# Kernel tuning notes

Measured on AMD Instinct MI355X. Metric: run time of the kernel, lower is better.

The kernel has to match this reference:

```python
import jax, jax.numpy as jnp
import numpy as np

NUM_HEADS = 8


def setup_inputs() -> dict:
    key = jax.random.key(0)
    ks = jax.random.split(key, 5)
    B, N, D = 2, 2048, 512
    scale = 1.0 / np.sqrt(D)  # xavier-ish init for stability
    return {
        "x": jax.random.normal(ks[0], (B, N, D), dtype=jnp.float32),
        "Wq": jax.random.normal(ks[1], (D, D), dtype=jnp.float32) * scale,
        "Wk": jax.random.normal(ks[2], (D, D), dtype=jnp.float32) * scale,
        "Wv": jax.random.normal(ks[3], (D, D), dtype=jnp.float32) * scale,
        "Wo": jax.random.normal(ks[4], (D, D), dtype=jnp.float32) * scale,
        "log_c": jnp.zeros((), dtype=jnp.float32),
        "log_beta": jnp.zeros((), dtype=jnp.float32),
    }


def reference(x, Wq, Wk, Wv, Wo, log_c, log_beta):
    B, N, D = x.shape
    H = NUM_HEADS
    dh = D // H

    # torch nn.Linear: y = x @ W.T
    def proj(W):
        return (x @ W.T).reshape(B, N, H, dh).transpose(0, 2, 1, 3)  # [B,H,N,dh]

    q, k, v = proj(Wq), proj(Wk), proj(Wv)

    c = jax.nn.softplus(log_c)
    beta = jax.nn.softplus(log_beta) + 0.5

    q_nsq = jnp.sum(q * q, axis=-1)  # [B,H,N]
    k_nsq = jnp.sum(k * k, axis=-1)  # [B,H,N]
    qk = jnp.einsum("bhnd,bhmd->bhnm", q, k)  # [B,H,N,N]

    diff_sq = jnp.maximum(q_nsq[..., :, None] - 2.0 * qk + k_nsq[..., None, :], 0.0)
    hyp_factor = jnp.sqrt(1.0 + c * (q_nsq[..., :, None] + k_nsq[..., None, :]))
    dist = jnp.sqrt(diff_sq + 1e-8) * hyp_factor
    scores = -beta * dist

    # causal mask (original: causal = mask is not None)
    causal = jnp.tril(jnp.ones((N, N), dtype=bool))
    scores = jnp.where(causal, scores, -jnp.inf)

    p = jax.nn.softmax(scores, axis=-1)
    out = jnp.einsum("bhnm,bhmd->bhnd", p, v)  # [B,H,N,dh]
    out = out.transpose(0, 2, 1, 3).reshape(B, N, D)
    return out @ Wo.T
```

## Files before the change

### kernel.cpp

```cpp
#include <hip/hip_runtime.h>
#include <math.h>

#define BB   2
#define NN   2048
#define DDIM 512
#define HH   8
#define DH   64
#define MTOT (BB*NN)
#define LDK  72
#define EE   (BB*HH*NN*DH)
#define WN   (DDIM*DDIM)
#define NSLOT (BB*HH*32*4)

typedef __attribute__((ext_vector_type(8))) short bf16x8;
typedef __attribute__((ext_vector_type(4))) float f32x4;

__device__ __forceinline__ float softplus_f(float x) {
    return x > 20.f ? x : log1pf(expf(x));
}
__device__ __forceinline__ unsigned short f2bf(float x) {
    union { float f; unsigned u; } v; v.f = x;
    unsigned r = v.u + 0x7fffu + ((v.u >> 16) & 1u);
    return (unsigned short)(r >> 16);
}
__device__ __forceinline__ float bf2f(unsigned short h) {
    union { unsigned u; float f; } v; v.u = ((unsigned)h) << 16; return v.f;
}

__global__ __launch_bounds__(256)
void split_hl(const float* __restrict__ x,  const float* __restrict__ Wq,
              const float* __restrict__ Wk, const float* __restrict__ Wv,
              const float* __restrict__ Wo,
              unsigned short* __restrict__ xh,  unsigned short* __restrict__ xl,
              unsigned short* __restrict__ wqh, unsigned short* __restrict__ wql,
              unsigned short* __restrict__ wkh, unsigned short* __restrict__ wkl,
              unsigned short* __restrict__ wvh, unsigned short* __restrict__ wvl,
              unsigned short* __restrict__ woh, unsigned short* __restrict__ wol)
{
    const float* src; unsigned short *dh, *dl; int nq;
    switch (blockIdx.y) {
        case 0:  src = x;  dh = xh;  dl = xl;  nq = EE / 4; break;
        case 1:  src = Wq; dh = wqh; dl = wql; nq = WN / 4; break;
        case 2:  src = Wk; dh = wkh; dl = wkl; nq = WN / 4; break;
        case 3:  src = Wv; dh = wvh; dl = wvl; nq = WN / 4; break;
        default: src = Wo; dh = woh; dl = wol; nq = WN / 4; break;
    }
    for (int i = blockIdx.x * 256 + threadIdx.x; i < nq; i += gridDim.x * 256) {
        float4 v = *(const float4*)(src + 4 * (size_t)i);
        ushort4 h, l;
        h.x = f2bf(v.x); l.x = f2bf(v.x - bf2f(h.x));
        h.y = f2bf(v.y); l.y = f2bf(v.y - bf2f(h.y));
        h.z = f2bf(v.z); l.z = f2bf(v.z - bf2f(h.z));
        h.w = f2bf(v.w); l.w = f2bf(v.w - bf2f(h.w));
        *(ushort4*)(dh + 4 * (size_t)i) = h;
        *(ushort4*)(dl + 4 * (size_t)i) = l;
    }
}

__global__ __launch_bounds__(256)
void mm_mfma(const unsigned short* __restrict__ Ahg, const unsigned short* __restrict__ Alg,
             const unsigned short* __restrict__ W0h, const unsigned short* __restrict__ W0l,
             const unsigned short* __restrict__ W1h, const unsigned short* __restrict__ W1l,
             const unsigned short* __restrict__ W2h, const unsigned short* __restrict__ W2l,
             const int is_out,
             unsigned short* __restrict__ Qhi, unsigned short* __restrict__ Qlo,
             unsigned short* __restrict__ Khi, unsigned short* __restrict__ Klo,
             unsigned short* __restrict__ Vb, float* __restrict__ Outp,
             float* __restrict__ QN, float* __restrict__ KN)
{
    const int mode = is_out ? 3 : (int)blockIdx.z;
    const unsigned short* Wh = (mode == 1) ? W1h : ((mode == 2) ? W2h : W0h);
    const unsigned short* Wl = (mode == 1) ? W1l : ((mode == 2) ? W2l : W0l);
    const int m0 = blockIdx.x * 128, n0 = blockIdx.y * 128;

    __shared__ unsigned short Ah_s[4 * 128 * 8];
    __shared__ unsigned short Al_s[4 * 128 * 8];
    __shared__ unsigned short Bh_s[4 * 128 * 8];
    __shared__ unsigned short Bl_s[4 * 128 * 8];

    const int tid  = threadIdx.x;
    const int lane = tid & 63, lx = lane & 15, q4 = lane >> 4;
    const int w = tid >> 6, wm = w & 1, wn = w >> 1;
    const int srow = tid & 127, skh = tid >> 7;

    f32x4 acc[4][4];
    #pragma unroll
    for (int mt = 0; mt < 4; ++mt)
        #pragma unroll
        for (int nt = 0; nt < 4; ++nt)
            acc[mt][nt] = (f32x4){0.f, 0.f, 0.f, 0.f};

    const int am = m0 + srow;
    const int ab = am >> 11, an = am & 2047;
    const size_t brow = (size_t)(n0 + srow) * DDIM;

    uint4 ra0, ra1, ra2, ra3, rb0, rb1, rb2, rb3;
    {
        const int e = skh * 16;
        size_t aoff = (mode == 3)
            ? ((((size_t)(ab * HH + (e >> 6)) * NN + an) << 6) + (e & 63))
            : ((size_t)am * DDIM + e);
        ra0 = *(const uint4*)(Ahg + aoff);     ra1 = *(const uint4*)(Ahg + aoff + 8);
        ra2 = *(const uint4*)(Alg + aoff);     ra3 = *(const uint4*)(Alg + aoff + 8);
        rb0 = *(const uint4*)(Wh + brow + e);  rb1 = *(const uint4*)(Wh + brow + e + 8);
        rb2 = *(const uint4*)(Wl + brow + e);  rb3 = *(const uint4*)(Wl + brow + e + 8);
    }

    for (int k0 = 0; k0 < DDIM; k0 += 32) {
        __syncthreads();
        const int kq = skh * 2;
        *(uint4*)&Ah_s[((kq + 0) * 128 + srow) * 8] = ra0;
        *(uint4*)&Ah_s[((kq + 1) * 128 + srow) * 8] = ra1;
        *(uint4*)&Al_s[((kq + 0) * 128 + srow) * 8] = ra2;
        *(uint4*)&Al_s[((kq + 1) * 128 + srow) * 8] = ra3;
        *(uint4*)&Bh_s[((kq + 0) * 128 + srow) * 8] = rb0;
        *(uint4*)&Bh_s[((kq + 1) * 128 + srow) * 8] = rb1;
        *(uint4*)&Bl_s[((kq + 0) * 128 + srow) * 8] = rb2;
        *(uint4*)&Bl_s[((kq + 1) * 128 + srow) * 8] = rb3;
        __syncthreads();

        if (k0 + 32 < DDIM) {
            const int e = k0 + 32 + skh * 16;
            size_t aoff = (mode == 3)
                ? ((((size_t)(ab * HH + (e >> 6)) * NN + an) << 6) + (e & 63))
                : ((size_t)am * DDIM + e);
            ra0 = *(const uint4*)(Ahg + aoff);     ra1 = *(const uint4*)(Ahg + aoff + 8);
            ra2 = *(const uint4*)(Alg + aoff);     ra3 = *(const uint4*)(Alg + aoff + 8);
            rb0 = *(const uint4*)(Wh + brow + e);  rb1 = *(const uint4*)(Wh + brow + e + 8);
            rb2 = *(const uint4*)(Wl + brow + e);  rb3 = *(const uint4*)(Wl + brow + e + 8);
        }

        bf16x8 fah[4], fal[4], fbh[4], fbl[4];
        #pragma unroll
        for (int t = 0; t < 4; ++t) {
            fah[t] = *(const bf16x8*)&Ah_s[(q4 * 128 + wm * 64 + t * 16 + lx) * 8];
            fal[t] = *(const bf16x8*)&Al_s[(q4 * 128 + wm * 64 + t * 16 + lx) * 8];
            fbh[t] = *(const bf16x8*)&Bh_s[(q4 * 128 + wn * 64 + t * 16 + lx) * 8];
            fbl[t] = *(const bf16x8*)&Bl_s[(q4 * 128 + wn * 64 + t * 16 + lx) * 8];
        }
        #pragma unroll
        for (int mt = 0; mt < 4; ++mt)
            #pragma unroll
            for (int nt = 0; nt < 4; ++nt) {
                acc[mt][nt] = __builtin_amdgcn_mfma_f32_16x16x32_bf16(fah[mt], fbh[nt], acc[mt][nt], 0, 0, 0);
                acc[mt][nt] = __builtin_amdgcn_mfma_f32_16x16x32_bf16(fah[mt], fbl[nt], acc[mt][nt], 0, 0, 0);
                acc[mt][nt] = __builtin_amdgcn_mfma_f32_16x16x32_bf16(fal[mt], fbh[nt], acc[mt][nt], 0, 0, 0);
            }
    }

    if (mode == 0 || mode == 1) {
        float* Np = (mode == 0) ? QN : KN;
        const int head = (n0 + wn * 64) >> 6;
        #pragma unroll
        for (int mt = 0; mt < 4; ++mt)
            #pragma unroll
            for (int r = 0; r < 4; ++r) {
                float s = 0.f;
                #pragma unroll
                for (int nt = 0; nt < 4; ++nt) s = fmaf(acc[mt][nt][r], acc[mt][nt][r], s);
                s += __shfl_xor(s, 1);
                s += __shfl_xor(s, 2);
                s += __shfl_xor(s, 4);
                s += __shfl_xor(s, 8);
                if (lx == 0) {
                    const int m = m0 + wm * 64 + mt * 16 + q4 * 4 + r;
                    Np[(size_t)((m >> 11) * HH + head) * NN + (m & 2047)] = s;
                }
            }
    }

    #pragma unroll
    for (int mt = 0; mt < 4; ++mt) {
        #pragma unroll
        for (int r = 0; r < 4; ++r) {
            const int m = m0 + wm * 64 + mt * 16 + q4 * 4 + r;
            const int b = m >> 11, n2 = m & 2047;
            #pragma unroll
            for (int nt = 0; nt < 4; ++nt) {
                const int j = n0 + wn * 64 + nt * 16 + lx;
                const float v = acc[mt][nt][r];
                if (mode == 3) {
                    Outp[(size_t)m * DDIM + j] = v;
                } else {
                    const size_t idx = (((size_t)(b * HH + (j >> 6)) * NN + n2) << 6) + (j & 63);
                    if (mode == 2) {
                        Vb[idx] = f2bf(v);
                    } else {
                        const unsigned short h = f2bf(v);
                        const unsigned short l = f2bf(v - bf2f(h));
                        if (mode == 0) { Qhi[idx] = h; Qlo[idx] = l; }
                        else           { Khi[idx] = h; Klo[idx] = l; }
                    }
                }
            }
        }
    }
}

__global__ __launch_bounds__(256)
void v_transpose(const unsigned short* __restrict__ Vb, unsigned short* __restrict__ Vt)
{
    __shared__ unsigned short T[64 * LDK];
    const int id = blockIdx.x;
    const int bh = id >> 5, nt = id & 31;
    const size_t ibase = (((size_t)bh * NN + nt * 64) << 6);
    const int row = threadIdx.x >> 2, ch = threadIdx.x & 3;

    #pragma unroll
    for (int half = 0; half < 2; ++half) {
        const int col = ch * 8 + half * 32;
        *(uint4*)&T[row * LDK + col] = *(const uint4*)(Vb + ibase + (row << 6) + col);
    }
    __syncthreads();

    const size_t obase = (size_t)bh * 64 * NN;
    #pragma unroll
    for (int half = 0; half < 2; ++half) {
        const int col = ch * 8 + half * 32;
        union { unsigned short u[8]; uint4 v; } tmp;
        #pragma unroll
        for (int j = 0; j < 8; ++j) tmp.u[j] = T[(col + j) * LDK + row];
        *(uint4*)(Vt + obase + (size_t)row * NN + nt * 64 + col) = tmp.v;
    }
}

__global__ __launch_bounds__(256, 2)
void attn_mfma(const unsigned short* __restrict__ Qhi, const unsigned short* __restrict__ Qlo,
               const unsigned short* __restrict__ Khi, const unsigned short* __restrict__ Klo,
               const unsigned short* __restrict__ Vt,
               const float* __restrict__ QN, const float* __restrict__ KN,
               const float* __restrict__ pLC, const float* __restrict__ pLB,
               float* __restrict__ Opart, float* __restrict__ Mp, float* __restrict__ Lp)
{
    __shared__ unsigned short Kh_s[64 * LDK];
    __shared__ unsigned short Kl_s[64 * LDK];
    __shared__ unsigned short Vt_s[64 * LDK];
    __shared__ unsigned short P_s [64 * LDK];
    __shared__ float kn_s[64];
    __shared__ float qn_s[64];

    const int idx = blockIdx.x;
    const int g   = (idx >= 48) ? 3 : (idx >= 24) ? 2 : (idx >= 8) ? 1 : 0;
    const int rem = idx - 4 * g * (g + 1);
    const int qt  = g * 8 + rem / (g + 1);
    const int c0  = rem % (g + 1);
    const int bh  = blockIdx.y;
    const int kt0 = c0 * 8;
    const int kend = min(kt0 + 8, qt + 1);

    const int tid  = threadIdx.x;
    const int w    = tid >> 6;
    const int lane = tid & 63;
    const int lx   = lane & 15;
    const int q4   = lane >> 4;

    const float hc   = softplus_f(pLC[0]);
    const float beta = softplus_f(pLB[0]) + 0.5f;

    const size_t base = ((size_t)bh * NN) << 6;

    const unsigned short* qrh = Qhi + base + ((size_t)(qt * 64 + w * 16 + lx) << 6) + q4 * 8;
    const unsigned short* qrl = Qlo + base + ((size_t)(qt * 64 + w * 16 + lx) << 6) + q4 * 8;
    const bf16x8 qh0 = *(const bf16x8*)(qrh);
    const bf16x8 qh1 = *(const bf16x8*)(qrh + 32);
    const bf16x8 ql0 = *(const bf16x8*)(qrl);
    const bf16x8 ql1 = *(const bf16x8*)(qrl + 32);

    if (tid < 64) qn_s[tid] = QN[(size_t)bh * NN + qt * 64 + tid];

    f32x4 Oacc[4];
    float m_st[4], l_st[4];
    #pragma unroll
    for (int r = 0; r < 4; ++r) {
        m_st[r] = -INFINITY; l_st[r] = 0.f;
        Oacc[r] = (f32x4){0.f, 0.f, 0.f, 0.f};
    }

    const int srow = tid >> 2, sch = tid & 3;

    uint4 pKh0, pKh1, pKl0, pKl1, pVt0, pVt1; float pkn = 0.f;
    {
        const unsigned short* kh = Khi + base + ((size_t)(kt0 * 64 + srow) << 6);
        const unsigned short* kl = Klo + base + ((size_t)(kt0 * 64 + srow) << 6);
        const unsigned short* vt = Vt  + base + (size_t)srow * NN + kt0 * 64;
        pKh0 = *(const uint4*)(kh + sch * 8);  pKh1 = *(const uint4*)(kh + sch * 8 + 32);
        pKl0 = *(const uint4*)(kl + sch * 8);  pKl1 = *(const uint4*)(kl + sch * 8 + 32);
        pVt0 = *(const uint4*)(vt + sch * 8);  pVt1 = *(const uint4*)(vt + sch * 8 + 32);
        if (tid < 64) pkn = KN[(size_t)bh * NN + kt0 * 64 + tid];
    }

    __syncthreads();

    for (int kt = kt0; kt < kend; ++kt) {
        *(uint4*)&Kh_s[srow * LDK + sch * 8]      = pKh0;
        *(uint4*)&Kh_s[srow * LDK + sch * 8 + 32] = pKh1;
        *(uint4*)&Kl_s[srow * LDK + sch * 8]      = pKl0;
        *(uint4*)&Kl_s[srow * LDK + sch * 8 + 32] = pKl1;
        *(uint4*)&Vt_s[srow * LDK + sch * 8]      = pVt0;
        *(uint4*)&Vt_s[srow * LDK + sch * 8 + 32] = pVt1;
        if (tid < 64) kn_s[tid] = pkn;
        __syncthreads();

        if (kt + 1 < kend) {
            const unsigned short* kh = Khi + base + ((size_t)((kt + 1) * 64 + srow) << 6);
            const unsigned short* kl = Klo + base + ((size_t)((kt + 1) * 64 + srow) << 6);
            const unsigned short* vt = Vt  + base + (size_t)srow * NN + (kt + 1) * 64;
            pKh0 = *(const uint4*)(kh + sch * 8);  pKh1 = *(const uint4*)(kh + sch * 8 + 32);
            pKl0 = *(const uint4*)(kl + sch * 8);  pKl1 = *(const uint4*)(kl + sch * 8 + 32);
            pVt0 = *(const uint4*)(vt + sch * 8);  pVt1 = *(const uint4*)(vt + sch * 8 + 32);
            if (tid < 64) pkn = KN[(size_t)bh * NN + (kt + 1) * 64 + tid];
        }

        f32x4 S[4];
        #pragma unroll
        for (int t = 0; t < 4; ++t) {
            f32x4 acc = (f32x4){0.f, 0.f, 0.f, 0.f};
            #pragma unroll
            for (int c2 = 0; c2 < 2; ++c2) {
                const int off = (t * 16 + lx) * LDK + c2 * 32 + q4 * 8;
                const bf16x8 kh = *(const bf16x8*)&Kh_s[off];
                const bf16x8 kl = *(const bf16x8*)&Kl_s[off];
                const bf16x8 qh = c2 ? qh1 : qh0;
                const bf16x8 ql = c2 ? ql1 : ql0;
                acc = __builtin_amdgcn_mfma_f32_16x16x32_bf16(qh, kh, acc, 0, 0, 0);
                acc = __builtin_amdgcn_mfma_f32_16x16x32_bf16(qh, kl, acc, 0, 0, 0);
                acc = __builtin_amdgcn_mfma_f32_16x16x32_bf16(ql, kh, acc, 0, 0, 0);
            }
            S[t] = acc;
        }

        float qn_r[4];
        #pragma unroll
        for (int r = 0; r < 4; ++r) qn_r[r] = qn_s[w * 16 + q4 * 4 + r];
        const bool diag = (kt == qt);

        float mrow[4] = {-INFINITY, -INFINITY, -INFINITY, -INFINITY};
        #pragma unroll
        for (int t = 0; t < 4; ++t) {
            const float kn = kn_s[t * 16 + lx];
            #pragma unroll
            for (int r = 0; r < 4; ++r) {
                const float sumn = qn_r[r] + kn;
                float diff = fmaxf(fmaf(-2.f, S[t][r], sumn), 0.f);
                float s = -beta * sqrtf(fmaf(hc, sumn, 1.f) * (diff + 1e-8f));
                const int cc = t * 16 + lx;
                const int rr = w * 16 + q4 * 4 + r;
                if (diag && cc > rr) s = -INFINITY;
                S[t][r] = s;
                mrow[r] = fmaxf(mrow[r], s);
            }
        }

        #pragma unroll
        for (int r = 0; r < 4; ++r) {
            float m = mrow[r];
            m = fmaxf(m, __shfl_xor(m, 1));
            m = fmaxf(m, __shfl_xor(m, 2));
            m = fmaxf(m, __shfl_xor(m, 4));
            m = fmaxf(m, __shfl_xor(m, 8));
            const float mn = fmaxf(m_st[r], m);
            const float al = __expf(m_st[r] - mn);
            m_st[r] = mn;
            float rs = 0.f;
            #pragma unroll
            for (int t = 0; t < 4; ++t) {
                const float p = __expf(S[t][r] - mn);
                rs += p;
                P_s[(w * 16 + q4 * 4 + r) * LDK + t * 16 + lx] = f2bf(p);
            }
            rs += __shfl_xor(rs, 1);
            rs += __shfl_xor(rs, 2);
            rs += __shfl_xor(rs, 4);
            rs += __shfl_xor(rs, 8);
            l_st[r] = l_st[r] * al + rs;
            #pragma unroll
            for (int t = 0; t < 4; ++t) Oacc[t][r] *= al;
        }

        __builtin_amdgcn_wave_barrier();

        #pragma unroll
        for (int c2 = 0; c2 < 2; ++c2) {
            const bf16x8 pa = *(const bf16x8*)&P_s[(w * 16 + lx) * LDK + c2 * 32 + q4 * 8];
            #pragma unroll
            for (int t = 0; t < 4; ++t) {
                const bf16x8 vb = *(const bf16x8*)&Vt_s[(t * 16 + lx) * LDK + c2 * 32 + q4 * 8];
                Oacc[t] = __builtin_amdgcn_mfma_f32_16x16x32_bf16(pa, vb, Oacc[t], 0, 0, 0);
            }
        }
        __syncthreads();
    }

    const int slot = ((bh * 32 + qt) << 2) + c0;
    float* op = Opart + ((size_t)slot << 12);
    #pragma unroll
    for (int r = 0; r < 4; ++r) {
        const int row = w * 16 + q4 * 4 + r;
        #pragma unroll
        for (int t = 0; t < 4; ++t)
            op[row * 64 + t * 16 + lx] = Oacc[t][r];
        if (lx == 0) {
            Mp[slot * 64 + row] = m_st[r];
            Lp[slot * 64 + row] = l_st[r];
        }
    }
}

__global__ __launch_bounds__(256)
void attn_combine(const float* __restrict__ Opart, const float* __restrict__ Mp,
                  const float* __restrict__ Lp,
                  unsigned short* __restrict__ AOh, unsigned short* __restrict__ AOl)
{
    const int bh = blockIdx.x >> 5, qt = blockIdx.x & 31;
    const int C = (qt >> 3) + 1;
    const int row = threadIdx.x >> 2, qd = threadIdx.x & 3;
    const int slot0 = (bh * 32 + qt) << 2;

    float m = -INFINITY;
    for (int c = 0; c < C; ++c) m = fmaxf(m, Mp[(slot0 + c) * 64 + row]);
    float L = 0.f;
    float o[16];
    #pragma unroll
    for (int j = 0; j < 16; ++j) o[j] = 0.f;

    for (int c = 0; c < C; ++c) {
        const float wgt = __expf(Mp[(slot0 + c) * 64 + row] - m);
        L += wgt * Lp[(slot0 + c) * 64 + row];
        const float* op = Opart + (((size_t)(slot0 + c)) << 12) + row * 64 + qd * 16;
        #pragma unroll
        for (int j4 = 0; j4 < 4; ++j4) {
            float4 v = *(const float4*)(op + j4 * 4);
            o[j4*4+0] = fmaf(wgt, v.x, o[j4*4+0]);
            o[j4*4+1] = fmaf(wgt, v.y, o[j4*4+1]);
            o[j4*4+2] = fmaf(wgt, v.z, o[j4*4+2]);
            o[j4*4+3] = fmaf(wgt, v.w, o[j4*4+3]);
        }
    }

    const float inv = 1.f / L;
    const size_t obase = (((size_t)bh * NN + qt * 64 + row) << 6) + qd * 16;
    union { unsigned short u[8]; uint4 v; } h2[2], l2[2];
    #pragma unroll
    for (int j = 0; j < 16; ++j) {
        const float ov = o[j] * inv;
        const unsigned short h = f2bf(ov);
        const unsigned short l = f2bf(ov - bf2f(h));
        h2[j >> 3].u[j & 7] = h;
        l2[j >> 3].u[j & 7] = l;
    }
    *(uint4*)(AOh + obase)     = h2[0].v;
    *(uint4*)(AOh + obase + 8) = h2[1].v;
    *(uint4*)(AOl + obase)     = l2[0].v;
    *(uint4*)(AOl + obase + 8) = l2[1].v;
}

extern "C" void kernel_launch(void* const* d_in, const int* in_sizes, int n_in,
                              void* d_out, int out_size, void* d_ws, size_t ws_size,
                              hipStream_t stream)
{
    const float* x        = (const float*)d_in[0];
    const float* Wq       = (const float*)d_in[1];
    const float* Wk       = (const float*)d_in[2];
    const float* Wv       = (const float*)d_in[3];
    const float* Wo       = (const float*)d_in[4];
    const float* log_c    = (const float*)d_in[5];
    const float* log_beta = (const float*)d_in[6];
    float* out = (float*)d_out;

    unsigned short* p = (unsigned short*)d_ws;
    unsigned short* xh  = p;            p += EE;
    unsigned short* xl  = p;            p += EE;
    unsigned short* wqh = p;            p += WN;
    unsigned short* wql = p;            p += WN;
    unsigned short* wkh = p;            p += WN;
    unsigned short* wkl = p;            p += WN;
    unsigned short* wvh = p;            p += WN;
    unsigned short* wvl = p;            p += WN;
    unsigned short* woh = p;            p += WN;
    unsigned short* wol = p;            p += WN;
    unsigned short* Qhi = p;            p += EE;
    unsigned short* Qlo = p;            p += EE;
    unsigned short* Khi = p;            p += EE;
    unsigned short* Klo = p;            p += EE;
    unsigned short* Vb  = p;            p += EE;
    unsigned short* Vtr = p;            p += EE;
    unsigned short* AOh = p;            p += EE;
    unsigned short* AOl = p;            p += EE;
    float* QN    = (float*)p;
    float* KN    = QN + (size_t)BB * HH * NN;
    float* Opart = KN + (size_t)BB * HH * NN;
    float* Mp    = Opart + (size_t)NSLOT * 64 * 64;
    float* Lp    = Mp + (size_t)NSLOT * 64;

    split_hl   <<<dim3(256, 5), 256, 0, stream>>>(x, Wq, Wk, Wv, Wo,
                                                  xh, xl, wqh, wql, wkh, wkl, wvh, wvl, woh, wol);
    mm_mfma    <<<dim3(MTOT / 128, 4, 3), 256, 0, stream>>>(xh, xl,
                                                  wqh, wql, wkh, wkl, wvh, wvl, 0,
                                                  Qhi, Qlo, Khi, Klo, Vb, nullptr, QN, KN);
    v_transpose<<<dim3(512), 256, 0, stream>>>(Vb, Vtr);
    attn_mfma  <<<dim3(80, 16), 256, 0, stream>>>(Qhi, Qlo, Khi, Klo, Vtr, QN, KN,
                                                  log_c, log_beta, Opart, Mp, Lp);
    attn_combine<<<dim3(512), 256, 0, stream>>>(Opart, Mp, Lp, AOh, AOl);
    mm_mfma    <<<dim3(MTOT / 128, 4, 1), 256, 0, stream>>>(AOh, AOl,
                                                  woh, wol, nullptr, nullptr, nullptr, nullptr, 1,
                                                  nullptr, nullptr, nullptr, nullptr, nullptr, out,
                                                  nullptr, nullptr);
}
```

Baseline: 217.8 us.

## Shrink GEMM M-tile, rebalance attention chunks, use MFMA row-sums and exp2

The projection GEMM tile is cut from 128 to 64 rows, doubling the grid and adding an occupancy hint, so more blocks are resident. Attention shared-memory tiles move from padded row-major to a k-chunked layout, key tiles are split evenly across causal chunks, and softmax uses exp2 with beta prescaled by log2(e). The per-row probability sum is now computed by an extra MFMA against a ones vector instead of shuffle reductions, and the attention occupancy hint rises from 2 to 4. Risks are that the P row sums come from bf16-rounded probabilities, and that the higher occupancy targets may force register spills.

```diff
diff --git a/kernel.cpp b/kernel.cpp
--- a/kernel.cpp
+++ b/kernel.cpp
@@ -57,7 +57,7 @@
     }
 }
 
-__global__ __launch_bounds__(256)
+__global__ __launch_bounds__(256, 3)
 void mm_mfma(const unsigned short* __restrict__ Ahg, const unsigned short* __restrict__ Alg,
              const unsigned short* __restrict__ W0h, const unsigned short* __restrict__ W0l,
              const unsigned short* __restrict__ W1h, const unsigned short* __restrict__ W1l,
@@ -71,75 +71,84 @@
     const int mode = is_out ? 3 : (int)blockIdx.z;
     const unsigned short* Wh = (mode == 1) ? W1h : ((mode == 2) ? W2h : W0h);
     const unsigned short* Wl = (mode == 1) ? W1l : ((mode == 2) ? W2l : W0l);
-    const int m0 = blockIdx.x * 128, n0 = blockIdx.y * 128;
-
-    __shared__ unsigned short Ah_s[4 * 128 * 8];
-    __shared__ unsigned short Al_s[4 * 128 * 8];
+    const int m0 = blockIdx.x * 64, n0 = blockIdx.y * 128;
+
+    __shared__ unsigned short Ah_s[4 * 64 * 8];
+    __shared__ unsigned short Al_s[4 * 64 * 8];
     __shared__ unsigned short Bh_s[4 * 128 * 8];
     __shared__ unsigned short Bl_s[4 * 128 * 8];
 
     const int tid  = threadIdx.x;
     const int lane = tid & 63, lx = lane & 15, q4 = lane >> 4;
     const int w = tid >> 6, wm = w & 1, wn = w >> 1;
-    const int srow = tid & 127, skh = tid >> 7;
-
-    f32x4 acc[4][4];
-    #pragma unroll
-    for (int mt = 0; mt < 4; ++mt)
+    const int rowA = tid & 63,  kqA = tid >> 6;
+    const int rowB = tid & 127, kb  = tid >> 7;
+
+    f32x4 acc[2][4];
+    #pragma unroll
+    for (int mt = 0; mt < 2; ++mt)
         #pragma unroll
         for (int nt = 0; nt < 4; ++nt)
             acc[mt][nt] = (f32x4){0.f, 0.f, 0.f, 0.f};
 
-    const int am = m0 + srow;
+    const int am = m0 + rowA;
     const int ab = am >> 11, an = am & 2047;
-    const size_t brow = (size_t)(n0 + srow) * DDIM;
-
-    uint4 ra0, ra1, ra2, ra3, rb0, rb1, rb2, rb3;
+    const size_t brow = (size_t)(n0 + rowB) * DDIM;
+
+    uint4 rah, ral, rbh0, rbh1, rbl0, rbl1;
     {
-        const int e = skh * 16;
+        const int e = kqA * 8;
         size_t aoff = (mode == 3)
             ? ((((size_t)(ab * HH + (e >> 6)) * NN + an) << 6) + (e & 63))
             : ((size_t)am * DDIM + e);
-        ra0 = *(const uint4*)(Ahg + aoff);     ra1 = *(const uint4*)(Ahg + aoff + 8);
-        ra2 = *(const uint4*)(Alg + aoff);     ra3 = *(const uint4*)(Alg + aoff + 8);
-        rb0 = *(const uint4*)(Wh + brow + e);  rb1 = *(const uint4*)(Wh + brow + e + 8);
-        rb2 = *(const uint4*)(Wl + brow + e);  rb3 = *(const uint4*)(Wl + brow + e + 8);
+        rah = *(const uint4*)(Ahg + aoff);
+        ral = *(const uint4*)(Alg + aoff);
+        const int eb = kb * 8;
+        rbh0 = *(const uint4*)(Wh + brow + eb);
+        rbh1 = *(const uint4*)(Wh + brow + eb + 16);
+        rbl0 = *(const uint4*)(Wl + brow + eb);
+        rbl1 = *(const uint4*)(Wl + brow + eb + 16);
     }
 
     for (int k0 = 0; k0 < DDIM; k0 += 32) {
         __syncthreads();
-        const int kq = skh * 2;
-        *(uint4*)&Ah_s[((kq + 0) * 128 + srow) * 8] = ra0;
-        *(uint4*)&Ah_s[((kq + 1) * 128 + srow) * 8] = ra1;
-        *(uint4*)&Al_s[((kq + 0) * 128 + srow) * 8] = ra2;
-        *(uint4*)&Al_s[((kq + 1) * 128 + srow) * 8] = ra3;
-        *(uint4*)&Bh_s[((kq + 0) * 128 + srow) * 8] = rb0;
-        *(uint4*)&Bh_s[((kq + 1) * 128 + srow) * 8] = rb1;
-        *(uint4*)&Bl_s[((kq + 0) * 128 + srow) * 8] = rb2;
-        *(uint4*)&Bl_s[((kq + 1) * 128 + srow) * 8] = rb3;
+        *(uint4*)&Ah_s[(kqA << 9) + (rowA << 3)] = rah;
+        *(uint4*)&Al_s[(kqA << 9) + (rowA << 3)] = ral;
+        *(uint4*)&Bh_s[(kb << 10) + (rowB << 3)]       = rbh0;
+        *(uint4*)&Bh_s[((kb + 2) << 10) + (rowB << 3)] = rbh1;
+        *(uint4*)&Bl_s[(kb << 10) + (rowB << 3)]       = rbl0;
+        *(uint4*)&Bl_s[((kb + 2) << 10) + (rowB << 3)] = rbl1;
         __syncthreads();
 
         if (k0 + 32 < DDIM) {
-            const int e = k0 + 32 + skh * 16;
+            const int e = k0 + 32 + kqA * 8;
             size_t aoff = (mode == 3)
                 ? ((((size_t)(ab * HH + (e >> 6)) * NN + an) << 6) + (e & 63))
                 : ((size_t)am * DDIM + e);
-            ra0 = *(const uint4*)(Ahg + aoff);     ra1 = *(const uint4*)(Ahg + aoff + 8);
-            ra2 = *(const uint4*)(Alg + aoff);     ra3 = *(const uint4*)(Alg + aoff + 8);
-            rb0 = *(const uint4*)(Wh + brow + e);  rb1 = *(const uint4*)(Wh + brow + e + 8);
-            rb2 = *(const uint4*)(Wl + brow + e);  rb3 = *(const uint4*)(Wl + brow + e + 8);
-        }
-
-        bf16x8 fah[4], fal[4], fbh[4], fbl[4];
-        #pragma unroll
-        for (int t = 0; t < 4; ++t) {
-            fah[t] = *(const bf16x8*)&Ah_s[(q4 * 128 + wm * 64 + t * 16 + lx) * 8];
-            fal[t] = *(const bf16x8*)&Al_s[(q4 * 128 + wm * 64 + t * 16 + lx) * 8];
-            fbh[t] = *(const bf16x8*)&Bh_s[(q4 * 128 + wn * 64 + t * 16 + lx) * 8];
-            fbl[t] = *(const bf16x8*)&Bl_s[(q4 * 128 + wn * 64 + t * 16 + lx) * 8];
-        }
-        #pragma unroll
-        for (int mt = 0; mt < 4; ++mt)
+            rah = *(const uint4*)(Ahg + aoff);
+            ral = *(const uint4*)(Alg + aoff);
+            const int eb = k0 + 32 + kb * 8;
+            rbh0 = *(const uint4*)(Wh + brow + eb);
+            rbh1 = *(const uint4*)(Wh + brow + eb + 16);
+            rbl0 = *(const uint4*)(Wl + brow + eb);
+            rbl1 = *(const uint4*)(Wl + brow + eb + 16);
+        }
+
+        bf16x8 fah[2], fal[2], fbh[4], fbl[4];
+        #pragma unroll
+        for (int mt = 0; mt < 2; ++mt) {
+            const int off = (q4 << 9) + ((wm * 32 + mt * 16 + lx) << 3);
+            fah[mt] = *(const bf16x8*)&Ah_s[off];
+            fal[mt] = *(const bf16x8*)&Al_s[off];
+        }
+        #pragma unroll
+        for (int nt = 0; nt < 4; ++nt) {
+            const int off = (q4 << 10) + ((wn * 64 + nt * 16 + lx) << 3);
+            fbh[nt] = *(const bf16x8*)&Bh_s[off];
+            fbl[nt] = *(const bf16x8*)&Bl_s[off];
+        }
+        #pragma unroll
+        for (int mt = 0; mt < 2; ++mt)
             #pragma unroll
             for (int nt = 0; nt < 4; ++nt) {
                 acc[mt][nt] = __builtin_amdgcn_mfma_f32_16x16x32_bf16(fah[mt], fbh[nt], acc[mt][nt], 0, 0, 0);
@@ -152,7 +161,7 @@
         float* Np = (mode == 0) ? QN : KN;
         const int head = (n0 + wn * 64) >> 6;
         #pragma unroll
-        for (int mt = 0; mt < 4; ++mt)
+        for (int mt = 0; mt < 2; ++mt)
             #pragma unroll
             for (int r = 0; r < 4; ++r) {
                 float s = 0.f;
@@ -163,17 +172,17 @@
                 s += __shfl_xor(s, 4);
                 s += __shfl_xor(s, 8);
                 if (lx == 0) {
-                    const int m = m0 + wm * 64 + mt * 16 + q4 * 4 + r;
+                    const int m = m0 + wm * 32 + mt * 16 + q4 * 4 + r;
                     Np[(size_t)((m >> 11) * HH + head) * NN + (m & 2047)] = s;
                 }
             }
     }
 
     #pragma unroll
-    for (int mt = 0; mt < 4; ++mt) {
+    for (int mt = 0; mt < 2; ++mt) {
         #pragma unroll
         for (int r = 0; r < 4; ++r) {
-            const int m = m0 + wm * 64 + mt * 16 + q4 * 4 + r;
+            const int m = m0 + wm * 32 + mt * 16 + q4 * 4 + r;
             const int b = m >> 11, n2 = m & 2047;
             #pragma unroll
             for (int nt = 0; nt < 4; ++nt) {
@@ -224,7 +233,7 @@
     }
 }
 
-__global__ __launch_bounds__(256, 2)
+__global__ __launch_bounds__(256, 4)
 void attn_mfma(const unsigned short* __restrict__ Qhi, const unsigned short* __restrict__ Qlo,
                const unsigned short* __restrict__ Khi, const unsigned short* __restrict__ Klo,
                const unsigned short* __restrict__ Vt,
@@ -232,21 +241,23 @@
                const float* __restrict__ pLC, const float* __restrict__ pLB,
                float* __restrict__ Opart, float* __restrict__ Mp, float* __restrict__ Lp)
 {
-    __shared__ unsigned short Kh_s[64 * LDK];
-    __shared__ unsigned short Kl_s[64 * LDK];
-    __shared__ unsigned short Vt_s[64 * LDK];
-    __shared__ unsigned short P_s [64 * LDK];
+    __shared__ unsigned short Kh_s[8 * 64 * 8];
+    __shared__ unsigned short Kl_s[8 * 64 * 8];
+    __shared__ unsigned short Vt_s[8 * 64 * 8];
+    __shared__ unsigned short P_s [8 * 64 * 8];
     __shared__ float kn_s[64];
     __shared__ float qn_s[64];
 
     const int idx = blockIdx.x;
     const int g   = (idx >= 48) ? 3 : (idx >= 24) ? 2 : (idx >= 8) ? 1 : 0;
     const int rem = idx - 4 * g * (g + 1);
-    const int qt  = g * 8 + rem / (g + 1);
-    const int c0  = rem % (g + 1);
+    const int C   = g + 1;
+    const int qt  = g * 8 + rem / C;
+    const int c0  = rem % C;
     const int bh  = blockIdx.y;
-    const int kt0 = c0 * 8;
-    const int kend = min(kt0 + 8, qt + 1);
+    const int nk  = qt + 1;
+    const int kt0  = (c0 * nk) / C;
+    const int kend = ((c0 + 1) * nk) / C;
 
     const int tid  = threadIdx.x;
     const int w    = tid >> 6;
@@ -254,10 +265,15 @@
     const int lx   = lane & 15;
     const int q4   = lane >> 4;
 
-    const float hc   = softplus_f(pLC[0]);
-    const float beta = softplus_f(pLB[0]) + 0.5f;
+    const float hc    = softplus_f(pLC[0]);
+    const float betaL = (softplus_f(pLB[0]) + 0.5f) * 1.44269504f;
 
     const size_t base = ((size_t)bh * NN) << 6;
+
+    union { unsigned short u[8]; bf16x8 v; } ones_u;
+    #pragma unroll
+    for (int j = 0; j < 8; ++j) ones_u.u[j] = 0x3F80;
+    const bf16x8 ones = ones_u.v;
 
     const unsigned short* qrh = Qhi + base + ((size_t)(qt * 64 + w * 16 + lx) << 6) + q4 * 8;
     const unsigned short* qrl = Qlo + base + ((size_t)(qt * 64 + w * 16 + lx) << 6) + q4 * 8;
@@ -269,10 +285,11 @@
     if (tid < 64) qn_s[tid] = QN[(size_t)bh * NN + qt * 64 + tid];
 
     f32x4 Oacc[4];
-    float m_st[4], l_st[4];
+    f32x4 Lacc = (f32x4){0.f, 0.f, 0.f, 0.f};
+    float m_st[4];
     #pragma unroll
     for (int r = 0; r < 4; ++r) {
-        m_st[r] = -INFINITY; l_st[r] = 0.f;
+        m_st[r] = -INFINITY;
         Oacc[r] = (f32x4){0.f, 0.f, 0.f, 0.f};
     }
 
@@ -292,12 +309,12 @@
     __syncthreads();
 
     for (int kt = kt0; kt < kend; ++kt) {
-        *(uint4*)&Kh_s[srow * LDK + sch * 8]      = pKh0;
-        *(uint4*)&Kh_s[srow * LDK + sch * 8 + 32] = pKh1;
-        *(uint4*)&Kl_s[srow * LDK + sch * 8]      = pKl0;
-        *(uint4*)&Kl_s[srow * LDK + sch * 8 + 32] = pKl1;
-        *(uint4*)&Vt_s[srow * LDK + sch * 8]      = pVt0;
-        *(uint4*)&Vt_s[srow * LDK + sch * 8 + 32] = pVt1;
+        *(uint4*)&Kh_s[(sch << 9) + (srow << 3)]       = pKh0;
+        *(uint4*)&Kh_s[((sch + 4) << 9) + (srow << 3)] = pKh1;
+        *(uint4*)&Kl_s[(sch << 9) + (srow << 3)]       = pKl0;
+        *(uint4*)&Kl_s[((sch + 4) << 9) + (srow << 3)] = pKl1;
+        *(uint4*)&Vt_s[(sch << 9) + (srow << 3)]       = pVt0;
+        *(uint4*)&Vt_s[((sch + 4) << 9) + (srow << 3)] = pVt1;
         if (tid < 64) kn_s[tid] = pkn;
         __syncthreads();
 
@@ -317,7 +334,7 @@
             f32x4 acc = (f32x4){0.f, 0.f, 0.f, 0.f};
             #pragma unroll
             for (int c2 = 0; c2 < 2; ++c2) {
-                const int off = (t * 16 + lx) * LDK + c2 * 32 + q4 * 8;
+                const int off = ((c2 * 4 + q4) << 9) + (t << 7) + (lx << 3);
                 const bf16x8 kh = *(const bf16x8*)&Kh_s[off];
                 const bf16x8 kl = *(const bf16x8*)&Kl_s[off];
                 const bf16x8 qh = c2 ? qh1 : qh0;
@@ -342,7 +359,7 @@
             for (int r = 0; r < 4; ++r) {
                 const float sumn = qn_r[r] + kn;
                 float diff = fmaxf(fmaf(-2.f, S[t][r], sumn), 0.f);
-                float s = -beta * sqrtf(fmaf(hc, sumn, 1.f) * (diff + 1e-8f));
+                float s = -betaL * sqrtf(fmaf(hc, sumn, 1.f) * (diff + 1e-8f));
                 const int cc = t * 16 + lx;
                 const int rr = w * 16 + q4 * 4 + r;
                 if (diag && cc > rr) s = -INFINITY;
@@ -359,34 +376,29 @@
             m = fmaxf(m, __shfl_xor(m, 4));
             m = fmaxf(m, __shfl_xor(m, 8));
             const float mn = fmaxf(m_st[r], m);
-            const float al = __expf(m_st[r] - mn);
+            const float al = exp2f(m_st[r] - mn);
             m_st[r] = mn;
-            float rs = 0.f;
+            const int prow = ((w * 16 + q4 * 4 + r) << 3) + (lx & 7);
             #pragma unroll
             for (int t = 0; t < 4; ++t) {
-                const float p = __expf(S[t][r] - mn);
-                rs += p;
-                P_s[(w * 16 + q4 * 4 + r) * LDK + t * 16 + lx] = f2bf(p);
-            }
-            rs += __shfl_xor(rs, 1);
-            rs += __shfl_xor(rs, 2);
-            rs += __shfl_xor(rs, 4);
-            rs += __shfl_xor(rs, 8);
-            l_st[r] = l_st[r] * al + rs;
-            #pragma unroll
-            for (int t = 0; t < 4; ++t) Oacc[t][r] *= al;
+                const float p = exp2f(S[t][r] - mn);
+                P_s[((t * 2 + (lx >> 3)) << 9) + prow] = f2bf(p);
+                Oacc[t][r] *= al;
+            }
+            Lacc[r] *= al;
         }
 
         __builtin_amdgcn_wave_barrier();
 
         #pragma unroll
         for (int c2 = 0; c2 < 2; ++c2) {
-            const bf16x8 pa = *(const bf16x8*)&P_s[(w * 16 + lx) * LDK + c2 * 32 + q4 * 8];
+            const bf16x8 pa = *(const bf16x8*)&P_s[((c2 * 4 + q4) << 9) + ((w * 16 + lx) << 3)];
             #pragma unroll
             for (int t = 0; t < 4; ++t) {
-                const bf16x8 vb = *(const bf16x8*)&Vt_s[(t * 16 + lx) * LDK + c2 * 32 + q4 * 8];
+                const bf16x8 vb = *(const bf16x8*)&Vt_s[((c2 * 4 + q4) << 9) + (t << 7) + (lx << 3)];
                 Oacc[t] = __builtin_amdgcn_mfma_f32_16x16x32_bf16(pa, vb, Oacc[t], 0, 0, 0);
             }
+            Lacc = __builtin_amdgcn_mfma_f32_16x16x32_bf16(pa, ones, Lacc, 0, 0, 0);
         }
         __syncthreads();
     }
@@ -401,7 +413,7 @@
             op[row * 64 + t * 16 + lx] = Oacc[t][r];
         if (lx == 0) {
             Mp[slot * 64 + row] = m_st[r];
-            Lp[slot * 64 + row] = l_st[r];
+            Lp[slot * 64 + row] = Lacc[r];
         }
     }
 }
@@ -424,7 +436,7 @@
     for (int j = 0; j < 16; ++j) o[j] = 0.f;
 
     for (int c = 0; c < C; ++c) {
-        const float wgt = __expf(Mp[(slot0 + c) * 64 + row] - m);
+        const float wgt = exp2f(Mp[(slot0 + c) * 64 + row] - m);
         L += wgt * Lp[(slot0 + c) * 64 + row];
         const float* op = Opart + (((size_t)(slot0 + c)) << 12) + row * 64 + qd * 16;
         #pragma unroll
@@ -494,14 +506,14 @@
 
     split_hl   <<<dim3(256, 5), 256, 0, stream>>>(x, Wq, Wk, Wv, Wo,
                                                   xh, xl, wqh, wql, wkh, wkl, wvh, wvl, woh, wol);
-    mm_mfma    <<<dim3(MTOT / 128, 4, 3), 256, 0, stream>>>(xh, xl,
+    mm_mfma    <<<dim3(MTOT / 64, 4, 3), 256, 0, stream>>>(xh, xl,
                                                   wqh, wql, wkh, wkl, wvh, wvl, 0,
                                                   Qhi, Qlo, Khi, Klo, Vb, nullptr, QN, KN);
     v_transpose<<<dim3(512), 256, 0, stream>>>(Vb, Vtr);
     attn_mfma  <<<dim3(80, 16), 256, 0, stream>>>(Qhi, Qlo, Khi, Klo, Vtr, QN, KN,
                                                   log_c, log_beta, Opart, Mp, Lp);
     attn_combine<<<dim3(512), 256, 0, stream>>>(Opart, Mp, Lp, AOh, AOl);
-    mm_mfma    <<<dim3(MTOT / 128, 4, 1), 256, 0, stream>>>(AOh, AOl,
+    mm_mfma    <<<dim3(MTOT / 64, 4, 1), 256, 0, stream>>>(AOh, AOl,
                                                   woh, wol, nullptr, nullptr, nullptr, nullptr, 1,
                                                   nullptr, nullptr, nullptr, nullptr, nullptr, out,
                                                   nullptr, nullptr);
```

Result: no change. 220.0 us (+1.0%).
